# Optimization experiments

Measured on AMD Instinct MI355X. Metric: run time of the kernel, lower is better.

## Reference

```python
import jax, jax.numpy as jnp
import numpy as np

WS = 7  # window size of the inner WindowAttention
EPS = 1e-5


def pc_roll(xb, shifts, axis):
    """Per-channel circular roll of [B,C,H,W] along `axis` (2 or 3).
    torch.roll semantics: out[i] = in[(i - shift) % n]."""
    n = xb.shape[axis]
    idx = (jnp.arange(n)[None, :] - shifts[:, None]) % n  # [C, n]
    if axis == 2:
        idxb = jnp.broadcast_to(idx[None, :, :, None], xb.shape)
    else:
        idxb = jnp.broadcast_to(idx[None, :, None, :], xb.shape)
    return jnp.take_along_axis(xb, idxb, axis=axis)


def layernorm(x, w, b):
    m = x.mean(-1, keepdims=True)
    v = x.var(-1, keepdims=True)
    return (x - m) * jax.lax.rsqrt(v + EPS) * w + b


def batchnorm2d(x, g, b):
    # training-mode BN: batch statistics over (B,H,W) per channel
    m = x.mean(axis=(0, 2, 3), keepdims=True)
    v = x.var(axis=(0, 2, 3), keepdims=True)
    return (x - m) * jax.lax.rsqrt(v + EPS) * g[None, :, None, None] + b[None, :, None, None]


def conv1x1(x, w, b):
    # x: [B,C,H,W], w: [Cout,Cin]
    return jnp.einsum('bchw,oc->bohw', x, w) + b[None, :, None, None]


def window_attention(q, k, v):
    # single-head Swin-style window attention, 7x7 windows, no rel-pos bias
    B, C, H, W = q.shape
    nh, nw = H // WS, W // WS

    def part(t):  # [B,C,H,W] -> [B*nh*nw, WS*WS, C]
        t = t.reshape(B, C, nh, WS, nw, WS)
        return t.transpose(0, 2, 4, 3, 5, 1).reshape(B * nh * nw, WS * WS, C)

    qw, kw, vw = part(q), part(k), part(v)
    scale = C ** -0.5
    attn = jax.nn.softmax(jnp.einsum('wnc,wmc->wnm', qw, kw) * scale, axis=-1)
    out = jnp.einsum('wnm,wmc->wnc', attn, vw)
    out = out.reshape(B, nh, nw, WS, WS, C).transpose(0, 5, 1, 3, 2, 4).reshape(B, C, H, W)
    return out


def setup_inputs() -> dict:
    B, H, W, C = 32, 56, 56, 128
    N = H * W
    key = jax.random.key(0)
    ks = jax.random.split(key, 16)
    f32 = jnp.float32

    def lin_w(k, din, dout):
        return 0.02 * jax.random.normal(k, (din, dout), dtype=f32)

    conv_std = float(np.sqrt(2.0 / C))
    inp = {
        'x': jax.random.normal(ks[0], (B, N, C), dtype=f32),
        'fc1_w': lin_w(ks[1], C, C), 'fc1_b': jnp.zeros((C,), f32),
        'fc2_w': lin_w(ks[2], C, C), 'fc2_b': jnp.zeros((C,), f32),
        'fc3_w': lin_w(ks[3], C, C), 'fc3_b': jnp.zeros((C,), f32),
        'fc4_w': lin_w(ks[4], C, C), 'fc4_b': jnp.zeros((C,), f32),
        'fc5_w': lin_w(ks[5], 2 * C, C), 'fc5_b': jnp.zeros((C,), f32),
        'fc6_w': lin_w(ks[6], 2 * C, C), 'fc6_b': jnp.zeros((C,), f32),
        'ln_w': jnp.ones((2 * C,), f32), 'ln_b': jnp.zeros((2 * C,), f32),
        'q_w': conv_std * jax.random.normal(ks[7], (C, C), dtype=f32), 'q_b': jnp.zeros((C,), f32),
        'k_w': conv_std * jax.random.normal(ks[8], (C, C), dtype=f32), 'k_b': jnp.zeros((C,), f32),
        'v_w': conv_std * jax.random.normal(ks[9], (C, C), dtype=f32), 'v_b': jnp.zeros((C,), f32),
        'bn1_g': jnp.ones((C,), f32), 'bn1_b': jnp.zeros((C,), f32),
        'bn2_g': jnp.ones((C,), f32), 'bn2_b': jnp.zeros((C,), f32),
        'H': H, 'W': W,
    }
    return inp


def reference(x, fc1_w, fc1_b, fc2_w, fc2_b, fc3_w, fc3_b, fc4_w, fc4_b,
              fc5_w, fc5_b, fc6_w, fc6_b, ln_w, ln_b,
              q_w, q_b, k_w, k_b, v_w, v_b, bn1_g, bn1_b, bn2_g, bn2_b, H, W):
    B, N, C = x.shape
    shifts = jnp.arange(C)
    gelu = lambda t: jax.nn.gelu(t, approximate=False)

    def to_bchw(t):
        return t.transpose(0, 2, 1).reshape(B, C, H, W)

    def to_bnc(t):
        return t.reshape(B, C, N).transpose(0, 2, 1)

    # branch 1: roll +c along H -> fc1 -> GELU -> roll +c along W -> fc2
    h = to_bnc(pc_roll(to_bchw(x), shifts, axis=2))
    h = gelu(h @ fc1_w + fc1_b)
    h = to_bnc(pc_roll(to_bchw(h), shifts, axis=3))
    x_1 = h @ fc2_w + fc2_b

    # branch 2: roll -c along W -> fc3 -> GELU -> roll +c along H -> fc4
    h = to_bnc(pc_roll(to_bchw(x), -shifts, axis=3))
    h = gelu(h @ fc3_w + fc3_b)
    h = to_bnc(pc_roll(to_bchw(h), shifts, axis=2))
    x_2 = h @ fc4_w + fc4_b

    x_1 = x_1 + x
    x_2 = x_2 + x
    x1 = jnp.concatenate([x_1, x_2], axis=2)          # [B,N,2C]
    x1 = layernorm(x1, ln_w, ln_b)
    x1 = x1 @ fc5_w + fc5_b
    x1 = x1 + x

    # local-attention branch (DWConv module actually runs WindowAtten + BN + ReLU)
    xb = to_bchw(x)
    att = window_attention(conv1x1(xb, q_w, q_b), conv1x1(xb, k_w, k_b), conv1x1(xb, v_w, v_b))
    x2 = jax.nn.relu(batchnorm2d(att, bn1_g, bn1_b))  # DWConv forward
    x2 = jax.nn.relu(x2)                              # act2 (idempotent, kept for fidelity)
    x2 = batchnorm2d(x2, bn2_g, bn2_b)                # norm2
    x2 = x2.reshape(B, C, N).transpose(0, 2, 1)       # [B,N,C]

    x3 = jnp.concatenate([x1, x2], axis=2)            # [B,N,2C]
    return x3 @ fc6_w + fc6_b
```

## Files before the change

kernel.cpp:

```cpp
#include <hip/hip_runtime.h>
#include <hip/hip_bf16.h>
#include <cstdint>
#include <cstddef>

typedef __bf16 bf16_t;
typedef __bf16 bf16x8 __attribute__((ext_vector_type(8)));
typedef float f32x4 __attribute__((ext_vector_type(4)));

#define B_SZ 32
#define H_SZ 56
#define W_SZ 56
#define N_TOK 3136
#define CH 128
#define M_TOT 100352

#define WOFF_FC1 0
#define WOFF_FC2 16384
#define WOFF_FC3 32768
#define WOFF_FC4 49152
#define WOFF_FC5 65536
#define WOFF_FC6 98304
#define WOFF_QW  131072
#define WOFF_KW  147456
#define WOFF_VW  163840
#define WTOT     180224

enum { A_FLAT = 0, A_WROLL, A_LN, A_BN };
enum { E_BIAS = 0, E_GELU, E_RES };

__device__ __forceinline__ float bf2f(bf16_t v) { return (float)v; }
__device__ __forceinline__ unsigned short bfbits(float v) {
    bf16_t b = (bf16_t)v; unsigned short u; __builtin_memcpy(&u, &b, 2); return u;
}
__device__ __forceinline__ int aswz(int row, int g) { return g ^ ((row >> 3) & 7); }

__global__ __launch_bounds__(256)
void wcvt_k(const float* __restrict__ f1, const float* __restrict__ f2,
            const float* __restrict__ f3, const float* __restrict__ f4,
            const float* __restrict__ f5, const float* __restrict__ f6,
            const float* __restrict__ qw, const float* __restrict__ kw,
            const float* __restrict__ vw, bf16_t* __restrict__ wb)
{
    const int blk = blockIdx.x;
    const int tid = threadIdx.x;
    if (blk < 32) {
        __shared__ bf16_t T[64][72];
        const float* src; bf16_t* dst; int K, t;
        if (blk < 4)       { src = f1; dst = wb + WOFF_FC1; K = 128; t = blk; }
        else if (blk < 8)  { src = f2; dst = wb + WOFF_FC2; K = 128; t = blk - 4; }
        else if (blk < 12) { src = f3; dst = wb + WOFF_FC3; K = 128; t = blk - 8; }
        else if (blk < 16) { src = f4; dst = wb + WOFF_FC4; K = 128; t = blk - 12; }
        else if (blk < 24) { src = f5; dst = wb + WOFF_FC5; K = 256; t = blk - 16; }
        else               { src = f6; dst = wb + WOFF_FC6; K = 256; t = blk - 24; }
        const int ti = t >> 1;
        const int tj = t & 1;
        for (int it = tid; it < 64 * 16; it += 256) {
            const int r = it >> 4, c4 = it & 15;
            float4 u = *(const float4*)(src + (size_t)(ti * 64 + r) * 128 + tj * 64 + c4 * 4);
            T[c4 * 4 + 0][r] = (bf16_t)u.x;
            T[c4 * 4 + 1][r] = (bf16_t)u.y;
            T[c4 * 4 + 2][r] = (bf16_t)u.z;
            T[c4 * 4 + 3][r] = (bf16_t)u.w;
        }
        __syncthreads();
        for (int it = tid; it < 64 * 8; it += 256) {
            const int n = it >> 3, ck = it & 7;
            *(uint4*)(dst + (size_t)(tj * 64 + n) * K + ti * 64 + ck * 8) =
                *(const uint4*)(&T[n][ck * 8]);
        }
    } else {
        const float* src; bf16_t* dst;
        int t = blk - 32;
        if (t < 4)      { src = qw; dst = wb + WOFF_QW; }
        else if (t < 8) { src = kw; dst = wb + WOFF_KW; t -= 4; }
        else            { src = vw; dst = wb + WOFF_VW; t -= 8; }
        const int base = t * 4096 + tid * 16;
        float4 u0 = *(const float4*)(src + base);
        float4 u1 = *(const float4*)(src + base + 4);
        float4 u2 = *(const float4*)(src + base + 8);
        float4 u3 = *(const float4*)(src + base + 12);
        bf16_t o[16] = {(bf16_t)u0.x, (bf16_t)u0.y, (bf16_t)u0.z, (bf16_t)u0.w,
                        (bf16_t)u1.x, (bf16_t)u1.y, (bf16_t)u1.z, (bf16_t)u1.w,
                        (bf16_t)u2.x, (bf16_t)u2.y, (bf16_t)u2.z, (bf16_t)u2.w,
                        (bf16_t)u3.x, (bf16_t)u3.y, (bf16_t)u3.z, (bf16_t)u3.w};
        *(uint4*)(dst + base) = *(const uint4*)o;
        *(uint4*)(dst + base + 8) = *(const uint4*)(o + 8);
    }
}

__global__ __launch_bounds__(256)
void transpose_k(const float* __restrict__ x, bf16_t* __restrict__ xT)
{
    __shared__ bf16_t T[128][70];
    const int tid = threadIdx.x;
    const int mbase = blockIdx.x * 64;
    const int bimg = mbase / N_TOK;
    const int n0 = mbase - bimg * N_TOK;
    for (int idx = tid; idx < 64 * 32; idx += 256) {
        const int tok = idx >> 5, cg = idx & 31;
        float4 u = *(const float4*)(x + (size_t)(mbase + tok) * CH + cg * 4);
        T[cg * 4 + 0][tok] = (bf16_t)u.x;
        T[cg * 4 + 1][tok] = (bf16_t)u.y;
        T[cg * 4 + 2][tok] = (bf16_t)u.z;
        T[cg * 4 + 3][tok] = (bf16_t)u.w;
    }
    __syncthreads();
    const uint* T32 = (const uint*)&T[0][0];
    for (int idx = tid; idx < 128 * 8; idx += 256) {
        const int c = idx >> 3, chunk = idx & 7;
        uint4 o;
        o.x = T32[c * 35 + chunk * 4 + 0];
        o.y = T32[c * 35 + chunk * 4 + 1];
        o.z = T32[c * 35 + chunk * 4 + 2];
        o.w = T32[c * 35 + chunk * 4 + 3];
        *(uint4*)(xT + ((size_t)(bimg * 128 + c)) * N_TOK + n0 + chunk * 8) = o;
    }
}

template<int AMODE, int KHALVES, int EPI, int WDIR, int OTRANS, int OF32>
__global__ __launch_bounds__(256)
void gemm_k(const bf16_t* __restrict__ A0, const bf16_t* __restrict__ A1,
            const bf16_t* __restrict__ Wt, const float* __restrict__ bias,
            const float* __restrict__ resid,
            const float* __restrict__ rowst,
            const float* __restrict__ lnw, const float* __restrict__ lnb,
            const float* __restrict__ bnp,
            void* __restrict__ outv)
{
    __shared__ __align__(16) char smem[17920];
    bf16_t* As = (bf16_t*)smem;
    const int tid = threadIdx.x;
    const int mbase = blockIdx.x * 64;
    const int bimg = mbase / N_TOK;
    const int n0 = mbase - bimg * N_TOK;
    const int lane = tid & 63;
    const int wv = tid >> 6;
    const int qd = lane >> 4;
    const int mr = lane & 15;
    const int KS = 128 * KHALVES;

    f32x4 acc[4][2];
#pragma unroll
    for (int i = 0; i < 4; ++i)
#pragma unroll
        for (int j = 0; j < 2; ++j) { f32x4 z = {0.f,0.f,0.f,0.f}; acc[i][j] = z; }

    for (int kh = 0; kh < KHALVES; ++kh) {
        if (kh) __syncthreads();
        if (AMODE == A_FLAT || AMODE == A_WROLL) {
            for (int idx = tid; idx < 128 * 8; idx += 256) {
                const int c = idx >> 3, chunk = idx & 7;
                const int cm = (c >= 112) ? c - 112 : (c >= 56 ? c - 56 : c);
                const bf16_t* crow = A0 + ((size_t)(bimg * 128 + c)) * N_TOK;
                const int cg = c >> 3, co = c & 7;
                if (AMODE == A_FLAT) {
                    int t = n0 + chunk * 8 + N_TOK - 56 * cm;
                    if (t >= N_TOK) t -= N_TOK;
                    uint4 u = *(const uint4*)(crow + t);
                    const bf16_t* up = (const bf16_t*)&u;
#pragma unroll
                    for (int j = 0; j < 8; ++j) {
                        const int row = chunk * 8 + j;
                        As[row * 136 + aswz(row, cg) * 8 + co] = up[j];
                    }
                } else {
                    const int nl = n0 + chunk * 8;
                    const int h = nl / 56;
                    const int w0 = nl - h * 56;
                    int ws = (WDIR > 0) ? (w0 + cm) : (w0 + 56 - cm);
                    if (ws >= 56) ws -= 56;
                    const bf16_t* hrow = crow + h * 56;
                    if (ws <= 48) {
                        uint4 u = *(const uint4*)(hrow + ws);
                        const bf16_t* up = (const bf16_t*)&u;
#pragma unroll
                        for (int j = 0; j < 8; ++j) {
                            const int row = chunk * 8 + j;
                            As[row * 136 + aswz(row, cg) * 8 + co] = up[j];
                        }
                    } else {
#pragma unroll
                        for (int j = 0; j < 8; ++j) {
                            int wj = ws + j; if (wj >= 56) wj -= 56;
                            const int row = chunk * 8 + j;
                            As[row * 136 + aswz(row, cg) * 8 + co] = hrow[wj];
                        }
                    }
                }
            }
        } else if (AMODE == A_LN) {
            for (int idx = tid; idx < 64 * 16; idx += 256) {
                const int row = idx >> 4, ck = idx & 15;
                const int rowg = mbase + row;
                const bf16_t* src = kh ? A1 : A0;
                uint4 u = *(const uint4*)(src + (size_t)rowg * CH + ck * 8);
                const bf16_t* up = (const bf16_t*)&u;
                const float mean = rowst[2 * rowg];
                const float rstd = rowst[2 * rowg + 1];
                const int cabs = kh * 128 + ck * 8;
                bf16_t t[8];
#pragma unroll
                for (int j = 0; j < 8; ++j) {
                    float v = (bf2f(up[j]) - mean) * rstd;
                    v = v * lnw[cabs + j] + lnb[cabs + j];
                    t[j] = (bf16_t)v;
                }
                *(uint4*)(&As[row * 136 + aswz(row, ck) * 8]) = *(const uint4*)t;
            }
        } else {
            for (int idx = tid; idx < 64 * 16; idx += 256) {
                const int row = idx >> 4, ck = idx & 15;
                const int rowg = mbase + row;
                if (kh == 0) {
                    uint4 u = *(const uint4*)(A0 + (size_t)rowg * CH + ck * 8);
                    *(uint4*)(&As[row * 136 + aswz(row, ck) * 8]) = u;
                } else {
                    uint4 u = *(const uint4*)(A1 + (size_t)rowg * CH + ck * 8);
                    const bf16_t* up = (const bf16_t*)&u;
                    bf16_t t[8];
#pragma unroll
                    for (int j = 0; j < 8; ++j) {
                        const int c = ck * 8 + j;
                        float z = fmaxf(0.f, bf2f(up[j]) * bnp[c] + bnp[128 + c]);
                        t[j] = (bf16_t)(z * bnp[256 + c] + bnp[384 + c]);
                    }
                    *(uint4*)(&As[row * 136 + aswz(row, ck) * 8]) = *(const uint4*)t;
                }
            }
        }
        __syncthreads();
        const bf16_t* wbase = Wt + (size_t)(wv * 32 + mr) * KS + kh * 128 + qd * 8;
#pragma unroll
        for (int kt = 0; kt < 4; ++kt) {
            bf16x8 af[4], bfr[2];
#pragma unroll
            for (int mt = 0; mt < 4; ++mt) {
                const int row = mt * 16 + mr;
                af[mt] = *(const bf16x8*)(&As[row * 136 + aswz(row, kt * 4 + qd) * 8]);
            }
#pragma unroll
            for (int nt = 0; nt < 2; ++nt)
                bfr[nt] = *(const bf16x8*)(wbase + (size_t)(nt * 16) * KS + kt * 32);
#pragma unroll
            for (int mt = 0; mt < 4; ++mt)
#pragma unroll
                for (int nt = 0; nt < 2; ++nt)
                    acc[mt][nt] = __builtin_amdgcn_mfma_f32_16x16x32_bf16(
                        af[mt], bfr[nt], acc[mt][nt], 0, 0, 0);
        }
    }
    if (OTRANS) {
        __syncthreads();
        uint* T32 = (uint*)smem;
#pragma unroll
        for (int mt = 0; mt < 4; ++mt)
#pragma unroll
            for (int nt = 0; nt < 2; ++nt) {
                const int col = wv * 32 + nt * 16 + mr;
                const float bb = bias[col];
#pragma unroll
                for (int rp = 0; rp < 2; ++rp) {
                    float v0 = acc[mt][nt][2 * rp] + bb;
                    float v1 = acc[mt][nt][2 * rp + 1] + bb;
                    if (EPI == E_GELU) {
                        v0 = 0.5f * v0 * (1.f + erff(v0 * 0.70710678118654752f));
                        v1 = 0.5f * v1 * (1.f + erff(v1 * 0.70710678118654752f));
                    }
                    T32[col * 35 + mt * 8 + qd * 2 + rp] =
                        (uint)bfbits(v0) | ((uint)bfbits(v1) << 16);
                }
            }
        __syncthreads();
        const int c = tid >> 1, half = tid & 1;
        uint r[16];
#pragma unroll
        for (int j = 0; j < 16; ++j) r[j] = T32[c * 35 + half * 16 + j];
        bf16_t* op = (bf16_t*)outv + ((size_t)(bimg * 128 + c)) * N_TOK + n0 + half * 32;
        uint4 o0 = {r[0], r[1], r[2], r[3]};
        uint4 o1 = {r[4], r[5], r[6], r[7]};
        uint4 o2 = {r[8], r[9], r[10], r[11]};
        uint4 o3 = {r[12], r[13], r[14], r[15]};
        ((uint4*)op)[0] = o0; ((uint4*)op)[1] = o1;
        ((uint4*)op)[2] = o2; ((uint4*)op)[3] = o3;
    } else {
#pragma unroll
        for (int mt = 0; mt < 4; ++mt)
#pragma unroll
            for (int nt = 0; nt < 2; ++nt) {
                const int col = wv * 32 + nt * 16 + mr;
                const float bb = bias[col];
#pragma unroll
                for (int r = 0; r < 4; ++r) {
                    const int rowg = mbase + mt * 16 + qd * 4 + r;
                    float v = acc[mt][nt][r] + bb;
                    if (EPI == E_GELU) v = 0.5f * v * (1.f + erff(v * 0.70710678118654752f));
                    if (EPI == E_RES)  v += resid[(size_t)rowg * CH + col];
                    if (OF32) ((float*)outv)[(size_t)rowg * CH + col] = v;
                    else ((bf16_t*)outv)[(size_t)rowg * CH + col] = (bf16_t)v;
                }
            }
    }
}

__global__ __launch_bounds__(256)
void qkv_k(const float* __restrict__ x, const bf16_t* __restrict__ wb,
           const float* __restrict__ qb, const float* __restrict__ kb,
           const float* __restrict__ vb,
           bf16_t* __restrict__ qo, bf16_t* __restrict__ ko, bf16_t* __restrict__ vo)
{
    __shared__ __align__(16) bf16_t As[64 * 136];
    const int tid = threadIdx.x;
    const int mbase = blockIdx.x * 64;
    const int lane = tid & 63;
    const int wv = tid >> 6;
    const int qd = lane >> 4;
    const int mr = lane & 15;

    for (int idx = tid; idx < 64 * 16; idx += 256) {
        const int row = idx >> 4, ck = idx & 15;
        const float* p = x + (size_t)(mbase + row) * CH + ck * 8;
        float4 u0 = *(const float4*)p;
        float4 u1 = *(const float4*)(p + 4);
        bf16_t t[8] = {(bf16_t)u0.x, (bf16_t)u0.y, (bf16_t)u0.z, (bf16_t)u0.w,
                       (bf16_t)u1.x, (bf16_t)u1.y, (bf16_t)u1.z, (bf16_t)u1.w};
        *(uint4*)(&As[row * 136 + aswz(row, ck) * 8]) = *(const uint4*)t;
    }
    __syncthreads();
    bf16x8 af[4][4];
#pragma unroll
    for (int kt = 0; kt < 4; ++kt)
#pragma unroll
        for (int mt = 0; mt < 4; ++mt) {
            const int row = mt * 16 + mr;
            af[kt][mt] = *(const bf16x8*)(&As[row * 136 + aswz(row, kt * 4 + qd) * 8]);
        }

    const int woffs[3] = {WOFF_QW, WOFF_KW, WOFF_VW};
    const float* bs3[3] = {qb, kb, vb};
    bf16_t* os3[3] = {qo, ko, vo};
#pragma unroll
    for (int s = 0; s < 3; ++s) {
        const bf16_t* wbase = wb + woffs[s] + (size_t)(wv * 32 + mr) * 128 + qd * 8;
        f32x4 acc[4][2];
#pragma unroll
        for (int i = 0; i < 4; ++i)
#pragma unroll
            for (int j = 0; j < 2; ++j) { f32x4 z = {0.f,0.f,0.f,0.f}; acc[i][j] = z; }
#pragma unroll
        for (int kt = 0; kt < 4; ++kt) {
            bf16x8 bfr[2];
#pragma unroll
            for (int nt = 0; nt < 2; ++nt)
                bfr[nt] = *(const bf16x8*)(wbase + (nt * 16) * 128 + kt * 32);
#pragma unroll
            for (int mt = 0; mt < 4; ++mt)
#pragma unroll
                for (int nt = 0; nt < 2; ++nt)
                    acc[mt][nt] = __builtin_amdgcn_mfma_f32_16x16x32_bf16(
                        af[kt][mt], bfr[nt], acc[mt][nt], 0, 0, 0);
        }
        bf16_t* out = os3[s];
#pragma unroll
        for (int mt = 0; mt < 4; ++mt)
#pragma unroll
            for (int nt = 0; nt < 2; ++nt) {
                const int col = wv * 32 + nt * 16 + mr;
                const float bb = bs3[s][col];
#pragma unroll
                for (int r = 0; r < 4; ++r) {
                    const int rowg = mbase + mt * 16 + qd * 4 + r;
                    out[(size_t)rowg * CH + col] = (bf16_t)(acc[mt][nt][r] + bb);
                }
            }
    }
}

__global__ __launch_bounds__(256)
void rowstats_k(const bf16_t* __restrict__ x1p, const bf16_t* __restrict__ x2p,
                float* __restrict__ rs)
{
    const int row = blockIdx.x * 4 + (threadIdx.x >> 6);
    const int lane = threadIdx.x & 63;
    const bf16_t* p1 = x1p + (size_t)row * CH + lane * 2;
    const bf16_t* p2 = x2p + (size_t)row * CH + lane * 2;
    float a0 = bf2f(p1[0]), a1 = bf2f(p1[1]);
    float b0 = bf2f(p2[0]), b1 = bf2f(p2[1]);
    float s = a0 + a1 + b0 + b1;
    float sq = a0 * a0 + a1 * a1 + b0 * b0 + b1 * b1;
#pragma unroll
    for (int off = 32; off > 0; off >>= 1) {
        s += __shfl_down(s, off);
        sq += __shfl_down(sq, off);
    }
    if (lane == 0) {
        float mean = s * (1.f / 256.f);
        float var = sq * (1.f / 256.f) - mean * mean;
        rs[2 * row] = mean;
        rs[2 * row + 1] = rsqrtf(var + 1e-5f);
    }
}

__global__ __launch_bounds__(256, 6)
void attn_k(const bf16_t* __restrict__ qg, const bf16_t* __restrict__ kg,
            const bf16_t* __restrict__ vg, bf16_t* __restrict__ og,
            float* __restrict__ partial)
{
    __shared__ __align__(16) char smem[27136];
    bf16_t* Vt = (bf16_t*)smem;
    bf16_t* Ps = (bf16_t*)(smem + 17408);
    float* bnacc = (float*)(smem + 26112);
    bf16_t* Os = (bf16_t*)smem;

    const int tid = threadIdx.x;
    const int blk = blockIdx.x;
    const int b = blk >> 6;
    const int wy = (blk >> 3) & 7;
    const int wx = blk & 7;
    const int lane = tid & 63;
    const int wv = tid >> 6;
    const int qd = lane >> 4;
    const int mr = lane & 15;

    bnacc[tid] = 0.f;

    const int vi0 = tid & 15;
    const int vck = tid >> 4;
    uint4 vld[4];
#pragma unroll
    for (int it = 0; it < 4; ++it) {
        const int i = vi0 + it * 16;
        uint4 uv = {0, 0, 0, 0};
        if (i < 49) {
            const int n = (wy * 7 + i / 7) * 56 + wx * 7 + (i % 7);
            uv = *(const uint4*)(vg + ((size_t)b * N_TOK + n) * CH + vck * 8);
        }
        vld[it] = uv;
    }

    const int qrow = wv * 16 + mr;
    const int qc = qrow < 49 ? qrow : 48;
    const bf16_t* qptr = qg + ((size_t)b * N_TOK +
                               (wy * 7 + qc / 7) * 56 + wx * 7 + (qc % 7)) * CH + qd * 8;
    bf16x8 aq[4];
#pragma unroll
    for (int kt = 0; kt < 4; ++kt)
        aq[kt] = *(const bf16x8*)(qptr + kt * 32);

    f32x4 sacc[4];
#pragma unroll
    for (int nt = 0; nt < 4; ++nt) {
        const int krow = nt * 16 + mr;
        const int kc = krow < 49 ? krow : 48;
        const bf16_t* kptr = kg + ((size_t)b * N_TOK +
                                   (wy * 7 + kc / 7) * 56 + wx * 7 + (kc % 7)) * CH + qd * 8;
        f32x4 a = {0.f, 0.f, 0.f, 0.f};
#pragma unroll
        for (int kt = 0; kt < 4; ++kt) {
            bf16x8 bk = *(const bf16x8*)(kptr + kt * 32);
            a = __builtin_amdgcn_mfma_f32_16x16x32_bf16(aq[kt], bk, a, 0, 0, 0);
        }
        sacc[nt] = a;
    }

#pragma unroll
    for (int it = 0; it < 4; ++it) {
        const int i = vi0 + it * 16;
        const bf16_t* vp = (const bf16_t*)&vld[it];
#pragma unroll
        for (int j = 0; j < 8; ++j)
            Vt[(vck * 8 + j) * 68 + i] = vp[j];
    }

    {
        const float SCALE = 0.088388347648318447f;
#pragma unroll
        for (int nt = 0; nt < 4; ++nt) {
            const bool bad = (nt * 16 + mr) > 48;
#pragma unroll
            for (int r = 0; r < 4; ++r)
                sacc[nt][r] = bad ? -1e30f : sacc[nt][r] * SCALE;
        }
        float pv[4][4];
        float inv[4];
#pragma unroll
        for (int r = 0; r < 4; ++r) {
            float m = fmaxf(fmaxf(sacc[0][r], sacc[1][r]), fmaxf(sacc[2][r], sacc[3][r]));
            m = fmaxf(m, __shfl_xor(m, 1));
            m = fmaxf(m, __shfl_xor(m, 2));
            m = fmaxf(m, __shfl_xor(m, 4));
            m = fmaxf(m, __shfl_xor(m, 8));
#pragma unroll
            for (int nt = 0; nt < 4; ++nt) pv[nt][r] = __expf(sacc[nt][r] - m);
            float s = (pv[0][r] + pv[1][r]) + (pv[2][r] + pv[3][r]);
            s += __shfl_xor(s, 1);
            s += __shfl_xor(s, 2);
            s += __shfl_xor(s, 4);
            s += __shfl_xor(s, 8);
            inv[r] = 1.f / s;
        }
#pragma unroll
        for (int nt = 0; nt < 4; ++nt)
#pragma unroll
            for (int r = 0; r < 4; ++r)
                Ps[(wv * 16 + qd * 4 + r) * 68 + nt * 16 + mr] = (bf16_t)(pv[nt][r] * inv[r]);
    }
    __syncthreads();

    bf16x8 ap[2];
    ap[0] = *(const bf16x8*)(&Ps[(wv * 16 + mr) * 68 + qd * 8]);
    ap[1] = *(const bf16x8*)(&Ps[(wv * 16 + mr) * 68 + 32 + qd * 8]);
    f32x4 oacc[8];
#pragma unroll
    for (int nt = 0; nt < 8; ++nt) {
        f32x4 a = {0.f, 0.f, 0.f, 0.f};
#pragma unroll
        for (int kt = 0; kt < 2; ++kt) {
            bf16x8 bv = *(const bf16x8*)(&Vt[(nt * 16 + mr) * 68 + kt * 32 + qd * 8]);
            a = __builtin_amdgcn_mfma_f32_16x16x32_bf16(ap[kt], bv, a, 0, 0, 0);
        }
        oacc[nt] = a;
    }

#pragma unroll
    for (int nt = 0; nt < 8; ++nt) {
        const int c = nt * 16 + mr;
        float s = 0.f, sq = 0.f;
#pragma unroll
        for (int r = 0; r < 4; ++r) {
            const int q = wv * 16 + qd * 4 + r;
            if (q < 49) { const float v = oacc[nt][r]; s += v; sq += v * v; }
        }
        s += __shfl_xor(s, 16); sq += __shfl_xor(sq, 16);
        s += __shfl_xor(s, 32); sq += __shfl_xor(sq, 32);
        if (qd == 0) { atomicAdd(&bnacc[c], s); atomicAdd(&bnacc[128 + c], sq); }
    }
    __syncthreads();

#pragma unroll
    for (int nt = 0; nt < 8; ++nt) {
        const int c = nt * 16 + mr;
#pragma unroll
        for (int r = 0; r < 4; ++r) {
            const int q = wv * 16 + qd * 4 + r;
            Os[q * 136 + c] = (bf16_t)oacc[nt][r];
        }
    }
    __syncthreads();

    for (int idx = tid; idx < 49 * 16; idx += 256) {
        const int row = idx >> 4, u = idx & 15;
        const int n = (wy * 7 + row / 7) * 56 + wx * 7 + (row % 7);
        *(uint4*)(og + ((size_t)b * N_TOK + n) * CH + u * 8) =
            *(const uint4*)(&Os[row * 136 + u * 8]);
    }
    partial[(size_t)blk * 256 + tid] = bnacc[tid];
}

__global__ __launch_bounds__(256)
void bnreduce_k(const float* __restrict__ partial, float* __restrict__ accum)
{
    const int t = threadIdx.x;
    const int r0 = blockIdx.x * 16;
    float s = 0.f;
#pragma unroll
    for (int r = 0; r < 16; ++r) s += partial[(size_t)(r0 + r) * 256 + t];
    atomicAdd(&accum[t], s);
}

__global__ __launch_bounds__(256)
void bnstats2_k(const bf16_t* __restrict__ att, const float* __restrict__ g1,
                const float* __restrict__ b1, float* __restrict__ accum)
{
    __shared__ float ls[256], lq[256];
    const int c = threadIdx.x & 127;
    const int half = threadIdx.x >> 7;
    const float m = accum[c] * (1.f / (float)M_TOT);
    const float var = accum[128 + c] * (1.f / (float)M_TOT) - m * m;
    const float rstd = rsqrtf(var + 1e-5f);
    const float scl = g1[c] * rstd;
    const float sh = b1[c] - m * scl;
    const size_t rowbase = (size_t)blockIdx.x * 196;
    float s = 0.f, sq = 0.f;
    for (int r = half; r < 196; r += 2) {
        float z = fmaxf(0.f, bf2f(att[(rowbase + r) * CH + c]) * scl + sh);
        s += z; sq += z * z;
    }
    ls[threadIdx.x] = s; lq[threadIdx.x] = sq;
    __syncthreads();
    if (threadIdx.x < 128) {
        atomicAdd(&accum[256 + c], ls[threadIdx.x] + ls[threadIdx.x + 128]);
        atomicAdd(&accum[384 + c], lq[threadIdx.x] + lq[threadIdx.x + 128]);
    }
}

__global__ void bnparams_k(const float* __restrict__ accum,
                           const float* __restrict__ g1, const float* __restrict__ b1,
                           const float* __restrict__ g2, const float* __restrict__ b2,
                           float* __restrict__ bnp)
{
    const int c = threadIdx.x;
    const float inv = 1.f / (float)M_TOT;
    float m1 = accum[c] * inv;
    float v1 = accum[128 + c] * inv - m1 * m1;
    float rs1 = rsqrtf(v1 + 1e-5f);
    float s1 = g1[c] * rs1;
    float sh1 = b1[c] - m1 * s1;
    float m2 = accum[256 + c] * inv;
    float v2 = accum[384 + c] * inv - m2 * m2;
    float rs2 = rsqrtf(v2 + 1e-5f);
    float s2 = g2[c] * rs2;
    float sh2 = b2[c] - m2 * s2;
    bnp[c] = s1; bnp[128 + c] = sh1; bnp[256 + c] = s2; bnp[384 + c] = sh2;
}

__global__ void zero_k(float* __restrict__ p) { p[threadIdx.x] = 0.f; }

extern "C" void kernel_launch(void* const* d_in, const int* in_sizes, int n_in,
                              void* d_out, int out_size, void* d_ws, size_t ws_size,
                              hipStream_t stream)
{
    (void)in_sizes; (void)n_in; (void)out_size; (void)ws_size;
    const float* x     = (const float*)d_in[0];
    const float* fc1_w = (const float*)d_in[1];
    const float* fc1_b = (const float*)d_in[2];
    const float* fc2_w = (const float*)d_in[3];
    const float* fc2_b = (const float*)d_in[4];
    const float* fc3_w = (const float*)d_in[5];
    const float* fc3_b = (const float*)d_in[6];
    const float* fc4_w = (const float*)d_in[7];
    const float* fc4_b = (const float*)d_in[8];
    const float* fc5_w = (const float*)d_in[9];
    const float* fc5_b = (const float*)d_in[10];
    const float* fc6_w = (const float*)d_in[11];
    const float* fc6_b = (const float*)d_in[12];
    const float* ln_w  = (const float*)d_in[13];
    const float* ln_b  = (const float*)d_in[14];
    const float* q_w   = (const float*)d_in[15];
    const float* q_b   = (const float*)d_in[16];
    const float* k_w   = (const float*)d_in[17];
    const float* k_b   = (const float*)d_in[18];
    const float* v_w   = (const float*)d_in[19];
    const float* v_b   = (const float*)d_in[20];
    const float* bn1_g = (const float*)d_in[21];
    const float* bn1_b = (const float*)d_in[22];
    const float* bn2_g = (const float*)d_in[23];
    const float* bn2_b = (const float*)d_in[24];

    char* ws = (char*)d_ws;
    const size_t SZB = (size_t)M_TOT * CH * sizeof(bf16_t);
    bf16_t* bufA = (bf16_t*)(ws);
    bf16_t* bufB = (bf16_t*)(ws + SZB);
    bf16_t* bufC = (bf16_t*)(ws + 2 * SZB);
    bf16_t* bufD = (bf16_t*)(ws + 3 * SZB);
    float*  rs   = (float*)(ws + 4 * SZB);
    float*  accum = (float*)(ws + 4 * SZB + (size_t)M_TOT * 2 * sizeof(float));
    float*  bnp  = accum + 512;
    float*  partial = bnp + 512;
    bf16_t* wbuf = (bf16_t*)(partial + 2048 * 256);

    const dim3 blk(256);
    const int GG = M_TOT / 64;

    zero_k<<<1, 512, 0, stream>>>(accum);
    wcvt_k<<<44, blk, 0, stream>>>(fc1_w, fc2_w, fc3_w, fc4_w, fc5_w, fc6_w,
                                   q_w, k_w, v_w, wbuf);
    transpose_k<<<GG, blk, 0, stream>>>(x, bufA);
    gemm_k<A_FLAT, 1, E_GELU, 0, 1, 0><<<GG, blk, 0, stream>>>(
        bufA, nullptr, wbuf + WOFF_FC1, fc1_b, nullptr, nullptr, nullptr, nullptr, nullptr, bufB);
    gemm_k<A_WROLL, 1, E_RES, -1, 0, 0><<<GG, blk, 0, stream>>>(
        bufB, nullptr, wbuf + WOFF_FC2, fc2_b, x, nullptr, nullptr, nullptr, nullptr, bufC);
    gemm_k<A_WROLL, 1, E_GELU, 1, 1, 0><<<GG, blk, 0, stream>>>(
        bufA, nullptr, wbuf + WOFF_FC3, fc3_b, nullptr, nullptr, nullptr, nullptr, nullptr, bufB);
    gemm_k<A_FLAT, 1, E_RES, 0, 0, 0><<<GG, blk, 0, stream>>>(
        bufB, nullptr, wbuf + WOFF_FC4, fc4_b, x, nullptr, nullptr, nullptr, nullptr, bufD);
    rowstats_k<<<M_TOT / 4, blk, 0, stream>>>(bufC, bufD, rs);
    gemm_k<A_LN, 2, E_RES, 0, 0, 0><<<GG, blk, 0, stream>>>(
        bufC, bufD, wbuf + WOFF_FC5, fc5_b, x, rs, ln_w, ln_b, nullptr, bufB);
    qkv_k<<<GG, blk, 0, stream>>>(x, wbuf, q_b, k_b, v_b, bufA, bufC, bufD);
    attn_k<<<B_SZ * 64, blk, 0, stream>>>(bufA, bufC, bufD, bufA, partial);
    bnreduce_k<<<128, blk, 0, stream>>>(partial, accum);
    bnstats2_k<<<512, blk, 0, stream>>>(bufA, bn1_g, bn1_b, accum);
    bnparams_k<<<1, 128, 0, stream>>>(accum, bn1_g, bn1_b, bn2_g, bn2_b, bnp);
    gemm_k<A_BN, 2, E_BIAS, 0, 0, 1><<<GG, blk, 0, stream>>>(
        bufB, bufA, wbuf + WOFF_FC6, fc6_b, nullptr, nullptr, nullptr, nullptr, bnp, d_out);
}
```

Before: 464.1 us.

## Stage window K tiles in LDS, drop A-tile XOR swizzle, hoist weight loads

In the window-attention kernel, K rows for the window are now loaded once, coalesced, into shared memory and read from there for QK^T. Before, each wave gathered K fragments straight from global memory with redundant strided loads. The V transpose and P store move after an extra barrier so the K buffer can alias the V region. The GEMM kernels drop the XOR swizzle on the A tile in favour of plain padded rows (stride 136), and hoist all four k-steps of weight fragment loads ahead of the MFMA loop. The added barrier and the unswizzled layout may bring LDS bank conflicts or sync stalls, and hoisting raises register pressure.

```diff
diff --git a/kernel.cpp b/kernel.cpp
--- a/kernel.cpp
+++ b/kernel.cpp
@@ -32,7 +32,6 @@
 __device__ __forceinline__ unsigned short bfbits(float v) {
     bf16_t b = (bf16_t)v; unsigned short u; __builtin_memcpy(&u, &b, 2); return u;
 }
-__device__ __forceinline__ int aswz(int row, int g) { return g ^ ((row >> 3) & 7); }
 
 __global__ __launch_bounds__(256)
 void wcvt_k(const float* __restrict__ f1, const float* __restrict__ f2,
@@ -152,17 +151,13 @@
                 const int c = idx >> 3, chunk = idx & 7;
                 const int cm = (c >= 112) ? c - 112 : (c >= 56 ? c - 56 : c);
                 const bf16_t* crow = A0 + ((size_t)(bimg * 128 + c)) * N_TOK;
-                const int cg = c >> 3, co = c & 7;
                 if (AMODE == A_FLAT) {
                     int t = n0 + chunk * 8 + N_TOK - 56 * cm;
                     if (t >= N_TOK) t -= N_TOK;
                     uint4 u = *(const uint4*)(crow + t);
                     const bf16_t* up = (const bf16_t*)&u;
 #pragma unroll
-                    for (int j = 0; j < 8; ++j) {
-                        const int row = chunk * 8 + j;
-                        As[row * 136 + aswz(row, cg) * 8 + co] = up[j];
-                    }
+                    for (int j = 0; j < 8; ++j) As[(chunk * 8 + j) * 136 + c] = up[j];
                 } else {
                     const int nl = n0 + chunk * 8;
                     const int h = nl / 56;
@@ -174,16 +169,12 @@
                         uint4 u = *(const uint4*)(hrow + ws);
                         const bf16_t* up = (const bf16_t*)&u;
 #pragma unroll
-                        for (int j = 0; j < 8; ++j) {
-                            const int row = chunk * 8 + j;
-                            As[row * 136 + aswz(row, cg) * 8 + co] = up[j];
-                        }
+                        for (int j = 0; j < 8; ++j) As[(chunk * 8 + j) * 136 + c] = up[j];
                     } else {
 #pragma unroll
                         for (int j = 0; j < 8; ++j) {
                             int wj = ws + j; if (wj >= 56) wj -= 56;
-                            const int row = chunk * 8 + j;
-                            As[row * 136 + aswz(row, cg) * 8 + co] = hrow[wj];
+                            As[(chunk * 8 + j) * 136 + c] = hrow[wj];
                         }
                     }
                 }
@@ -205,7 +196,7 @@
                     v = v * lnw[cabs + j] + lnb[cabs + j];
                     t[j] = (bf16_t)v;
                 }
-                *(uint4*)(&As[row * 136 + aswz(row, ck) * 8]) = *(const uint4*)t;
+                *(uint4*)(&As[row * 136 + ck * 8]) = *(const uint4*)t;
             }
         } else {
             for (int idx = tid; idx < 64 * 16; idx += 256) {
@@ -213,7 +204,7 @@
                 const int rowg = mbase + row;
                 if (kh == 0) {
                     uint4 u = *(const uint4*)(A0 + (size_t)rowg * CH + ck * 8);
-                    *(uint4*)(&As[row * 136 + aswz(row, ck) * 8]) = u;
+                    *(uint4*)(&As[row * 136 + ck * 8]) = u;
                 } else {
                     uint4 u = *(const uint4*)(A1 + (size_t)rowg * CH + ck * 8);
                     const bf16_t* up = (const bf16_t*)&u;
@@ -224,29 +215,30 @@
                         float z = fmaxf(0.f, bf2f(up[j]) * bnp[c] + bnp[128 + c]);
                         t[j] = (bf16_t)(z * bnp[256 + c] + bnp[384 + c]);
                     }
-                    *(uint4*)(&As[row * 136 + aswz(row, ck) * 8]) = *(const uint4*)t;
+                    *(uint4*)(&As[row * 136 + ck * 8]) = *(const uint4*)t;
                 }
             }
         }
         __syncthreads();
         const bf16_t* wbase = Wt + (size_t)(wv * 32 + mr) * KS + kh * 128 + qd * 8;
+        bf16x8 bfr[4][2];
+#pragma unroll
+        for (int kt = 0; kt < 4; ++kt)
+#pragma unroll
+            for (int nt = 0; nt < 2; ++nt)
+                bfr[kt][nt] = *(const bf16x8*)(wbase + (size_t)(nt * 16) * KS + kt * 32);
 #pragma unroll
         for (int kt = 0; kt < 4; ++kt) {
-            bf16x8 af[4], bfr[2];
-#pragma unroll
-            for (int mt = 0; mt < 4; ++mt) {
-                const int row = mt * 16 + mr;
-                af[mt] = *(const bf16x8*)(&As[row * 136 + aswz(row, kt * 4 + qd) * 8]);
-            }
-#pragma unroll
-            for (int nt = 0; nt < 2; ++nt)
-                bfr[nt] = *(const bf16x8*)(wbase + (size_t)(nt * 16) * KS + kt * 32);
+            bf16x8 af[4];
+#pragma unroll
+            for (int mt = 0; mt < 4; ++mt)
+                af[mt] = *(const bf16x8*)(&As[(mt * 16 + mr) * 136 + kt * 32 + qd * 8]);
 #pragma unroll
             for (int mt = 0; mt < 4; ++mt)
 #pragma unroll
                 for (int nt = 0; nt < 2; ++nt)
                     acc[mt][nt] = __builtin_amdgcn_mfma_f32_16x16x32_bf16(
-                        af[mt], bfr[nt], acc[mt][nt], 0, 0, 0);
+                        af[mt], bfr[kt][nt], acc[mt][nt], 0, 0, 0);
         }
     }
     if (OTRANS) {
@@ -323,17 +315,15 @@
         float4 u1 = *(const float4*)(p + 4);
         bf16_t t[8] = {(bf16_t)u0.x, (bf16_t)u0.y, (bf16_t)u0.z, (bf16_t)u0.w,
                        (bf16_t)u1.x, (bf16_t)u1.y, (bf16_t)u1.z, (bf16_t)u1.w};
-        *(uint4*)(&As[row * 136 + aswz(row, ck) * 8]) = *(const uint4*)t;
+        *(uint4*)(&As[row * 136 + ck * 8]) = *(const uint4*)t;
     }
     __syncthreads();
     bf16x8 af[4][4];
 #pragma unroll
     for (int kt = 0; kt < 4; ++kt)
 #pragma unroll
-        for (int mt = 0; mt < 4; ++mt) {
-            const int row = mt * 16 + mr;
-            af[kt][mt] = *(const bf16x8*)(&As[row * 136 + aswz(row, kt * 4 + qd) * 8]);
-        }
+        for (int mt = 0; mt < 4; ++mt)
+            af[kt][mt] = *(const bf16x8*)(&As[(mt * 16 + mr) * 136 + kt * 32 + qd * 8]);
 
     const int woffs[3] = {WOFF_QW, WOFF_KW, WOFF_VW};
     const float* bs3[3] = {qb, kb, vb};
@@ -406,6 +396,7 @@
             float* __restrict__ partial)
 {
     __shared__ __align__(16) char smem[27136];
+    bf16_t* Kr = (bf16_t*)smem;
     bf16_t* Vt = (bf16_t*)smem;
     bf16_t* Ps = (bf16_t*)(smem + 17408);
     float* bnacc = (float*)(smem + 26112);
@@ -423,6 +414,20 @@
 
     bnacc[tid] = 0.f;
 
+    const int kck = tid & 15;
+    const int kt0 = tid >> 4;
+    uint4 kld[4];
+#pragma unroll
+    for (int it = 0; it < 4; ++it) {
+        const int i = kt0 + it * 16;
+        uint4 u = {0, 0, 0, 0};
+        if (i < 49) {
+            const int n = (wy * 7 + i / 7) * 56 + wx * 7 + (i % 7);
+            u = *(const uint4*)(kg + ((size_t)b * N_TOK + n) * CH + kck * 8);
+        }
+        kld[it] = u;
+    }
+
     const int vi0 = tid & 15;
     const int vck = tid >> 4;
     uint4 vld[4];
@@ -446,31 +451,25 @@
     for (int kt = 0; kt < 4; ++kt)
         aq[kt] = *(const bf16x8*)(qptr + kt * 32);
 
+#pragma unroll
+    for (int it = 0; it < 4; ++it)
+        *(uint4*)(&Kr[(kt0 + it * 16) * 132 + kck * 8]) = kld[it];
+    __syncthreads();
+
     f32x4 sacc[4];
 #pragma unroll
     for (int nt = 0; nt < 4; ++nt) {
-        const int krow = nt * 16 + mr;
-        const int kc = krow < 49 ? krow : 48;
-        const bf16_t* kptr = kg + ((size_t)b * N_TOK +
-                                   (wy * 7 + kc / 7) * 56 + wx * 7 + (kc % 7)) * CH + qd * 8;
         f32x4 a = {0.f, 0.f, 0.f, 0.f};
 #pragma unroll
         for (int kt = 0; kt < 4; ++kt) {
-            bf16x8 bk = *(const bf16x8*)(kptr + kt * 32);
+            bf16x8 bk = *(const bf16x8*)(&Kr[(nt * 16 + mr) * 132 + kt * 32 + qd * 8]);
             a = __builtin_amdgcn_mfma_f32_16x16x32_bf16(aq[kt], bk, a, 0, 0, 0);
         }
         sacc[nt] = a;
     }
 
-#pragma unroll
-    for (int it = 0; it < 4; ++it) {
-        const int i = vi0 + it * 16;
-        const bf16_t* vp = (const bf16_t*)&vld[it];
-#pragma unroll
-        for (int j = 0; j < 8; ++j)
-            Vt[(vck * 8 + j) * 68 + i] = vp[j];
-    }
-
+    float pv[4][4];
+    float inv[4];
     {
         const float SCALE = 0.088388347648318447f;
 #pragma unroll
@@ -480,8 +479,6 @@
             for (int r = 0; r < 4; ++r)
                 sacc[nt][r] = bad ? -1e30f : sacc[nt][r] * SCALE;
         }
-        float pv[4][4];
-        float inv[4];
 #pragma unroll
         for (int r = 0; r < 4; ++r) {
             float m = fmaxf(fmaxf(sacc[0][r], sacc[1][r]), fmaxf(sacc[2][r], sacc[3][r]));
@@ -498,12 +495,22 @@
             s += __shfl_xor(s, 8);
             inv[r] = 1.f / s;
         }
-#pragma unroll
-        for (int nt = 0; nt < 4; ++nt)
-#pragma unroll
-            for (int r = 0; r < 4; ++r)
-                Ps[(wv * 16 + qd * 4 + r) * 68 + nt * 16 + mr] = (bf16_t)(pv[nt][r] * inv[r]);
-    }
+    }
+    __syncthreads();
+
+#pragma unroll
+    for (int it = 0; it < 4; ++it) {
+        const int i = vi0 + it * 16;
+        const bf16_t* vp = (const bf16_t*)&vld[it];
+#pragma unroll
+        for (int j = 0; j < 8; ++j)
+            Vt[(vck * 8 + j) * 68 + i] = vp[j];
+    }
+#pragma unroll
+    for (int nt = 0; nt < 4; ++nt)
+#pragma unroll
+        for (int r = 0; r < 4; ++r)
+            Ps[(wv * 16 + qd * 4 + r) * 68 + nt * 16 + mr] = (bf16_t)(pv[nt][r] * inv[r]);
     __syncthreads();
 
     bf16x8 ap[2];
```

Measured after the change: 467.1 us. About the same (+0.7%).
